# Kernel tuning notes

Measured on AMD Instinct MI355X. Metric: run time of the kernel, lower is better.

Reference implementation:

```python
import jax, jax.numpy as jnp
import numpy as np
from jax import lax

STRIDE = (1, 1)
PADDING = ((1, 1), (1, 1))
DILATION = (1, 1)


def setup_inputs() -> dict:
    key = jax.random.key(0)
    k1, k2, k3, k4 = jax.random.split(key, 4)
    bs, cin, h, w = 64, 128, 56, 56
    k_exp, cout, kh, kw = 8, 128, 3, 3
    x = jax.random.normal(k1, (bs, cin, h, w), dtype=jnp.float32)
    routing_weight = jax.random.uniform(k2, (bs, k_exp), dtype=jnp.float32)
    weight = jax.random.normal(k3, (k_exp, cout, cin, kh, kw), dtype=jnp.float32) * (1.0 / np.sqrt(cin * kh * kw))
    bias = jax.random.normal(k4, (k_exp, cout), dtype=jnp.float32) * 0.01
    return {"x": x, "routing_weight": routing_weight, "weight": weight, "bias": bias}


def reference(x, routing_weight, weight, bias):
    # CondConv combine_kernel path: per-sample kernel = routing-weighted sum of experts,
    # then a standard conv per sample (equivalent to torch groups=bs trick).
    # w_mix: [bs, oc, c, kh, kw]
    w_mix = jnp.einsum('bk,kocij->bocij', routing_weight, weight)
    b_mix = routing_weight @ bias  # [bs, oc]

    def conv_one(xi, wi):
        # xi: [c, h, w], wi: [oc, c, kh, kw]
        return lax.conv_general_dilated(
            xi[None], wi,
            window_strides=STRIDE,
            padding=PADDING,
            rhs_dilation=DILATION,
            dimension_numbers=('NCHW', 'OIHW', 'NCHW'),
        )[0]  # [oc, oh, ow]

    out = jax.vmap(conv_one)(x, w_mix)  # [bs, oc, oh, ow]
    out = out + b_mix[:, :, None, None]
    return out
```

## Files before the change

### kernel.cpp

```cpp
#include <hip/hip_runtime.h>

#define BS    64
#define CIN   128
#define OCH   128
#define HW    56
#define KEXP  8
#define KTOT  1152
#define NSTEP 36
#define PLANEC 3364
#define WMIX_PS (NSTEP * OCH * 32)
#define TPAD  60

typedef __bf16 bf16x8 __attribute__((ext_vector_type(8)));
typedef __bf16 bf16x4 __attribute__((ext_vector_type(4)));
typedef float  f32x4  __attribute__((ext_vector_type(4)));

__device__ __forceinline__ unsigned f2bf(float f) {
    union { float f; unsigned u; } v; v.f = f;
    unsigned r = v.u + 0x7fffu + ((v.u >> 16) & 1u);
    return r >> 16;
}

__device__ __forceinline__ void gl16(const unsigned short* g, unsigned short* l) {
    __builtin_amdgcn_global_load_lds(
        (const __attribute__((address_space(1))) void*)g,
        (__attribute__((address_space(3))) void*)l, 16, 0, 0);
}

__global__ __launch_bounds__(256) void prep_xt(const float* __restrict__ x,
                                               unsigned short* __restrict__ xt) {
    __shared__ unsigned short t[CIN * TPAD];
    int b = blockIdx.x, ihp = blockIdx.y;
    int tid = threadIdx.x;
    bool border = (ihp == 0) || (ihp == 57);
    if (!border) {
        int ih = ihp - 1;
        const float* xr = x + (size_t)b * CIN * HW * HW + (size_t)ih * HW;
        #pragma unroll
        for (int i7 = 0; i7 < 7; ++i7) {
            int i = i7 * 256 + tid;
            int c = i / 14, w4 = i - c * 14;
            float4 v = *(const float4*)(xr + (size_t)c * (HW * HW) + w4 * 4);
            bf16x4 pk = { (__bf16)v.x, (__bf16)v.y, (__bf16)v.z, (__bf16)v.w };
            *(bf16x4*)&t[c * TPAD + w4 * 4] = pk;
        }
    }
    __syncthreads();
    for (int j = tid; j < 928; j += 256) {
        int qq = j / 232, rr = j - qq * 232;
        int oct = rr / 58, col = rr - oct * 58;
        union { unsigned short u[8]; uint4 v; } o;
        o.v = make_uint4(0u, 0u, 0u, 0u);
        if (!border && col >= 1 && col <= 56) {
            #pragma unroll
            for (int k = 0; k < 8; ++k)
                o.u[k] = t[(qq * 32 + oct * 8 + k) * TPAD + (col - 1)];
        }
        *(uint4*)&xt[(((size_t)(b * 16 + qq * 4 + oct)) * PLANEC
                      + (size_t)ihp * 58 + col) * 8] = o.v;
    }
}

__global__ __launch_bounds__(256) void prep_wmix(
        const float* __restrict__ rw, const float* __restrict__ wgt,
        const float* __restrict__ bias,
        unsigned short* __restrict__ wmix, float* __restrict__ bmix) {
    __shared__ float wlds[KEXP * KTOT];
    __shared__ float rwl[16 * KEXP];
    int oc  = blockIdx.x;
    int bg  = blockIdx.y;
    int tid = threadIdx.x;

    if (tid < 16 * KEXP) rwl[tid] = rw[bg * 16 * KEXP + tid];
    const float* wsrc = wgt + (size_t)oc * KTOT;
    #pragma unroll
    for (int e = 0; e < KEXP; ++e) {
        const float* we = wsrc + (size_t)e * OCH * KTOT;
        for (int j = tid; j < KTOT; j += 256) wlds[e * KTOT + j] = we[j];
    }
    __syncthreads();

    if (tid < 16) {
        float a = 0.f;
        #pragma unroll
        for (int e = 0; e < KEXP; ++e) a += rwl[tid * KEXP + e] * bias[e * OCH + oc];
        bmix[(size_t)(bg * 16 + tid) * OCH + oc] = a;
    }

    for (int t = tid; t < KTOT; t += 256) {
        int c = t & 127, rs = t >> 7;
        int q = c >> 5, cl = c & 31;
        size_t oidx = ((size_t)(q * 9 + rs) * OCH + oc) * 32 + cl;
        float w8[KEXP];
        #pragma unroll
        for (int e = 0; e < KEXP; ++e) w8[e] = wlds[e * KTOT + c * 9 + rs];
        #pragma unroll
        for (int b = 0; b < 16; ++b) {
            float a = 0.f;
            #pragma unroll
            for (int e = 0; e < KEXP; ++e) a += rwl[b * KEXP + e] * w8[e];
            wmix[(size_t)(bg * 16 + b) * WMIX_PS + oidx] = (unsigned short)f2bf(a);
        }
    }
}

__global__ __launch_bounds__(128, 2) void condconv_mfma(
        const unsigned short* __restrict__ xt, const unsigned short* __restrict__ wmix,
        const float* __restrict__ bmix, float* __restrict__ out) {
    __shared__ unsigned short patch[2][8192];

    int blk  = blockIdx.x;
    int b    = blk & 63;
    int tile = blk >> 6;
    int oh0  = tile * 2;
    int tid  = threadIdx.x;
    int wave = tid >> 6, lane = tid & 63, ln = lane & 15, quad = lane >> 4;

    const unsigned short* ap = wmix + (size_t)b * WMIX_PS
                             + (size_t)(wave * 64 + ln) * 32 + quad * 8;

    const unsigned short* xb = xt + (size_t)(b * 16) * (PLANEC * 8)
                             + (size_t)oh0 * 58 * 8;

    int rcl[8], octl[8];
    #pragma unroll
    for (int i = 0; i < 8; ++i) {
        int rc = (i & 3) * 64 + lane;
        rcl[i]  = (rc > 231) ? 231 : rc;
        octl[i] = 2 * wave + (i >> 2);
    }

    int cb[7], offn[7];
    #pragma unroll
    for (int nt = 0; nt < 7; ++nt) {
        int n   = nt * 16 + ln;
        int row = (n >= 56) ? 1 : 0;
        int ow  = n - row * 56;
        cb[nt]   = (quad * 256 + row * 58 + ow) * 8;
        offn[nt] = (oh0 + row) * HW + ow;
    }

    f32x4 acc[4][7] = {};

    auto stage = [&](int qq, int bf) {
        #pragma unroll
        for (int i = 0; i < 8; ++i) {
            const unsigned short* src = xb
                + ((size_t)(qq * 4 + octl[i]) * PLANEC + rcl[i]) * 8;
            gl16(src, &patch[bf][wave * 4096 + i * 512]);
        }
    };

    stage(0, 0);
    bf16x8 pa[2][4];
    #pragma unroll
    for (int mt = 0; mt < 4; ++mt) {
        pa[0][mt] = *(const bf16x8*)(ap + mt * 512);
        pa[1][mt] = *(const bf16x8*)(ap + 4096 + mt * 512);
    }
    __syncthreads();

    #pragma unroll
    for (int qq = 0; qq < 4; ++qq) {
        if (qq < 3) stage(qq + 1, (qq + 1) & 1);
        #pragma unroll
        for (int s9 = 0; s9 < 9; ++s9) {
            const int s = qq * 9 + s9;
            bf16x8 ca[4];
            #pragma unroll
            for (int mt = 0; mt < 4; ++mt) ca[mt] = pa[s & 1][mt];
            const int sp = (s + 2 < NSTEP) ? (s + 2) : (NSTEP - 1);
            #pragma unroll
            for (int mt = 0; mt < 4; ++mt)
                pa[s & 1][mt] = *(const bf16x8*)(ap + (size_t)sp * 4096 + mt * 512);
            const int r = s9 / 3, sc = s9 - r * 3;
            const int pshift = (r * 58 + sc) * 8;
            #pragma unroll
            for (int nt = 0; nt < 7; ++nt) {
                bf16x8 bb = *(const bf16x8*)&patch[qq & 1][cb[nt] + pshift];
                acc[0][nt] = __builtin_amdgcn_mfma_f32_16x16x32_bf16(ca[0], bb, acc[0][nt], 0, 0, 0);
                acc[1][nt] = __builtin_amdgcn_mfma_f32_16x16x32_bf16(ca[1], bb, acc[1][nt], 0, 0, 0);
                acc[2][nt] = __builtin_amdgcn_mfma_f32_16x16x32_bf16(ca[2], bb, acc[2][nt], 0, 0, 0);
                acc[3][nt] = __builtin_amdgcn_mfma_f32_16x16x32_bf16(ca[3], bb, acc[3][nt], 0, 0, 0);
            }
        }
        __syncthreads();
    }

    const float* bmb = bmix + b * OCH;
    float* ob = out + (size_t)b * OCH * HW * HW;
    #pragma unroll
    for (int mt = 0; mt < 4; ++mt) {
        #pragma unroll
        for (int rg = 0; rg < 4; ++rg) {
            int oc = wave * 64 + mt * 16 + quad * 4 + rg;
            float bv = bmb[oc];
            #pragma unroll
            for (int nt = 0; nt < 7; ++nt)
                ob[(size_t)oc * (HW * HW) + offn[nt]] = acc[mt][nt][rg] + bv;
        }
    }
}

extern "C" void kernel_launch(void* const* d_in, const int* in_sizes, int n_in,
                              void* d_out, int out_size, void* d_ws, size_t ws_size,
                              hipStream_t stream) {
    (void)in_sizes; (void)n_in; (void)out_size; (void)ws_size;
    const float* x    = (const float*)d_in[0];
    const float* rw   = (const float*)d_in[1];
    const float* wgt  = (const float*)d_in[2];
    const float* bias = (const float*)d_in[3];
    float* outp = (float*)d_out;

    unsigned short* wmix = (unsigned short*)d_ws;
    float* bmix = (float*)((char*)d_ws + (size_t)BS * WMIX_PS * 2);
    unsigned short* xtw = (unsigned short*)((char*)d_ws + (size_t)BS * WMIX_PS * 2 + 32768);

    hipLaunchKernelGGL(prep_xt,   dim3(BS, 58), dim3(256), 0, stream, x, xtw);
    hipLaunchKernelGGL(prep_wmix, dim3(OCH, 4), dim3(256), 0, stream, rw, wgt, bias, wmix, bmix);
    hipLaunchKernelGGL(condconv_mfma, dim3(BS * 28), dim3(128), 0, stream,
                       xtw, wmix, bmix, outp);
}
```

Before: 274.9 us.

## Split output tile across four waves in a 2x2 layout

The main conv kernel moves from 2 waves to 4 waves per block. Waves are arranged as 2 along output channels and 2 along pixels, and each wave handles 4 pixel tiles instead of 7. The pixel split overlaps: both halves compute tile 3, and the second half skips storing it. This cuts accumulator registers per wave and raises occupancy (launch bounds 256,3). In exchange it duplicates one pixel tile of MFMA work and loads each weight fragment in two waves.

New measurement: 298.7 us. 8.7% more time.

```diff
diff --git a/kernel.cpp b/kernel.cpp
--- a/kernel.cpp
+++ b/kernel.cpp
@@ -104,7 +104,7 @@
     }
 }
 
-__global__ __launch_bounds__(128, 2) void condconv_mfma(
+__global__ __launch_bounds__(256, 3) void condconv_mfma(
         const unsigned short* __restrict__ xt, const unsigned short* __restrict__ wmix,
         const float* __restrict__ bmix, float* __restrict__ out) {
     __shared__ unsigned short patch[2][8192];
@@ -115,40 +115,38 @@
     int oh0  = tile * 2;
     int tid  = threadIdx.x;
     int wave = tid >> 6, lane = tid & 63, ln = lane & 15, quad = lane >> 4;
+    int wm = wave & 1, wn = wave >> 1;
 
     const unsigned short* ap = wmix + (size_t)b * WMIX_PS
-                             + (size_t)(wave * 64 + ln) * 32 + quad * 8;
+                             + (size_t)(wm * 64 + ln) * 32 + quad * 8;
 
     const unsigned short* xb = xt + (size_t)(b * 16) * (PLANEC * 8)
                              + (size_t)oh0 * 58 * 8;
 
-    int rcl[8], octl[8];
-    #pragma unroll
-    for (int i = 0; i < 8; ++i) {
-        int rc = (i & 3) * 64 + lane;
-        rcl[i]  = (rc > 231) ? 231 : rc;
-        octl[i] = 2 * wave + (i >> 2);
-    }
-
-    int cb[7], offn[7];
-    #pragma unroll
-    for (int nt = 0; nt < 7; ++nt) {
-        int n   = nt * 16 + ln;
+    int rcl[4];
+    #pragma unroll
+    for (int i = 0; i < 4; ++i) {
+        int rc = i * 64 + lane;
+        rcl[i] = (rc > 231) ? 231 : rc;
+    }
+
+    int cb[4], offn[4];
+    #pragma unroll
+    for (int j = 0; j < 4; ++j) {
+        int n   = (wn * 3 + j) * 16 + ln;
         int row = (n >= 56) ? 1 : 0;
         int ow  = n - row * 56;
-        cb[nt]   = (quad * 256 + row * 58 + ow) * 8;
-        offn[nt] = (oh0 + row) * HW + ow;
-    }
-
-    f32x4 acc[4][7] = {};
+        cb[j]   = (quad * 256 + row * 58 + ow) * 8;
+        offn[j] = (oh0 + row) * HW + ow;
+    }
+
+    f32x4 acc[4][4] = {};
 
     auto stage = [&](int qq, int bf) {
-        #pragma unroll
-        for (int i = 0; i < 8; ++i) {
-            const unsigned short* src = xb
-                + ((size_t)(qq * 4 + octl[i]) * PLANEC + rcl[i]) * 8;
-            gl16(src, &patch[bf][wave * 4096 + i * 512]);
-        }
+        const unsigned short* sq = xb + (size_t)(qq * 4 + wave) * (PLANEC * 8);
+        #pragma unroll
+        for (int i = 0; i < 4; ++i)
+            gl16(sq + (size_t)rcl[i] * 8, &patch[bf][(wave * 256 + i * 64) * 8]);
     };
 
     stage(0, 0);
@@ -176,12 +174,12 @@
             const int r = s9 / 3, sc = s9 - r * 3;
             const int pshift = (r * 58 + sc) * 8;
             #pragma unroll
-            for (int nt = 0; nt < 7; ++nt) {
-                bf16x8 bb = *(const bf16x8*)&patch[qq & 1][cb[nt] + pshift];
-                acc[0][nt] = __builtin_amdgcn_mfma_f32_16x16x32_bf16(ca[0], bb, acc[0][nt], 0, 0, 0);
-                acc[1][nt] = __builtin_amdgcn_mfma_f32_16x16x32_bf16(ca[1], bb, acc[1][nt], 0, 0, 0);
-                acc[2][nt] = __builtin_amdgcn_mfma_f32_16x16x32_bf16(ca[2], bb, acc[2][nt], 0, 0, 0);
-                acc[3][nt] = __builtin_amdgcn_mfma_f32_16x16x32_bf16(ca[3], bb, acc[3][nt], 0, 0, 0);
+            for (int j = 0; j < 4; ++j) {
+                bf16x8 bb = *(const bf16x8*)&patch[qq & 1][cb[j] + pshift];
+                acc[0][j] = __builtin_amdgcn_mfma_f32_16x16x32_bf16(ca[0], bb, acc[0][j], 0, 0, 0);
+                acc[1][j] = __builtin_amdgcn_mfma_f32_16x16x32_bf16(ca[1], bb, acc[1][j], 0, 0, 0);
+                acc[2][j] = __builtin_amdgcn_mfma_f32_16x16x32_bf16(ca[2], bb, acc[2][j], 0, 0, 0);
+                acc[3][j] = __builtin_amdgcn_mfma_f32_16x16x32_bf16(ca[3], bb, acc[3][j], 0, 0, 0);
             }
         }
         __syncthreads();
@@ -193,11 +191,13 @@
     for (int mt = 0; mt < 4; ++mt) {
         #pragma unroll
         for (int rg = 0; rg < 4; ++rg) {
-            int oc = wave * 64 + mt * 16 + quad * 4 + rg;
+            int oc = wm * 64 + mt * 16 + quad * 4 + rg;
             float bv = bmb[oc];
             #pragma unroll
-            for (int nt = 0; nt < 7; ++nt)
-                ob[(size_t)oc * (HW * HW) + offn[nt]] = acc[mt][nt][rg] + bv;
+            for (int j = 0; j < 4; ++j) {
+                if (wn == 1 && j == 0) continue;
+                ob[(size_t)oc * (HW * HW) + offn[j]] = acc[mt][j][rg] + bv;
+            }
         }
     }
 }
@@ -218,6 +218,6 @@
 
     hipLaunchKernelGGL(prep_xt,   dim3(BS, 58), dim3(256), 0, stream, x, xtw);
     hipLaunchKernelGGL(prep_wmix, dim3(OCH, 4), dim3(256), 0, stream, rw, wgt, bias, wmix, bmix);
-    hipLaunchKernelGGL(condconv_mfma, dim3(BS * 28), dim3(128), 0, stream,
+    hipLaunchKernelGGL(condconv_mfma, dim3(BS * 28), dim3(256), 0, stream,
                        xtw, wmix, bmix, outp);
 }
```
